# Optimization experiments

Hardware: AMD Instinct MI355X
Metric: run time of the kernel (lower is better)

The kernel has to match this reference:

```python
import jax, jax.numpy as jnp
import numpy as np

B = 4096
MAX_ATOMS = 2048  # angles_max_length + 1
EPS = 1e-12


def setup_inputs() -> dict:
    key = jax.random.key(0)
    k1, k2, k3 = jax.random.split(key, 3)
    inp = jax.random.normal(k1, (B, 3 * MAX_ATOMS), dtype=jnp.float32)
    tgt = jax.random.normal(k2, (B, 3 * MAX_ATOMS), dtype=jnp.float32)
    lengths = jax.random.randint(k3, (B,), 1, 2047, dtype=jnp.int32)
    return {"input": inp, "target": tgt, "angles_length": lengths}


def _kabsch_rmsd(inp, tgt, angles_length):
    # [B, 3*N] flat xyz -> [B, N, 3]
    b, three_n = inp.shape
    n_atoms_max = three_n // 3
    x = inp.reshape(b, n_atoms_max, 3)
    y = tgt.reshape(b, n_atoms_max, 3)
    # number of valid atoms per sample = angles_length + 1
    n_valid = (angles_length + 1).astype(x.dtype)  # [B]
    mask = (jnp.arange(n_atoms_max)[None, :] < (angles_length[:, None] + 1))
    mask = mask.astype(x.dtype)[..., None]  # [B, N, 1]
    # masked centroids
    denom = n_valid[:, None, None]
    cx = (x * mask).sum(axis=1, keepdims=True) / denom
    cy = (y * mask).sum(axis=1, keepdims=True) / denom
    xc = (x - cx) * mask
    yc = (y - cy) * mask
    # sum of squared norms of both centered point sets
    ssq = (xc * xc).sum(axis=(1, 2)) + (yc * yc).sum(axis=(1, 2))  # [B]
    # 3x3 cross-covariance per sample
    C = jnp.einsum('bni,bnj->bij', xc, yc)  # [B, 3, 3]
    U, S, Vt = jnp.linalg.svd(C)
    # Kabsch det correction (proper rotation)
    d = jnp.sign(jnp.linalg.det(U) * jnp.linalg.det(Vt))  # [B]
    tr = S[:, 0] + S[:, 1] + d * S[:, 2]
    msd = jnp.maximum(ssq - 2.0 * tr, 0.0) / n_valid
    return jnp.sqrt(msd + EPS)


def reference(input, target, angles_length):
    return _kabsch_rmsd(input, target, angles_length)
```

## Files before the change

kernel.cpp:

```cpp
#include <hip/hip_runtime.h>
#include <math.h>


#define NACC 17
#define ROWF 6144

__global__ __launch_bounds__(256) void kabsch_moments_kernel(
    const float* __restrict__ X,
    const float* __restrict__ Y,
    const int* __restrict__ L,
    float* __restrict__ WS,
    int B)
{
    const int gwave = (int)((blockIdx.x * 256u + threadIdx.x) >> 6);
    const int lane  = threadIdx.x & 63;
    if (gwave >= B) return;
    const int row = gwave;
    const int n = L[row] + 1;
    const int nIter = (n + 255) >> 8;

    const float* gX = X + (size_t)row * ROWF + (size_t)lane * 12;
    const float* gY = Y + (size_t)row * ROWF + (size_t)lane * 12;

    float v[NACC];
#pragma unroll
    for (int k = 0; k < NACC; ++k) v[k] = 0.0f;

    float4 cx0, cx1, cx2, cy0, cy1, cy2;
    {
        const float4* px = (const float4*)gX;
        const float4* py = (const float4*)gY;
        cx0 = px[0]; cx1 = px[1]; cx2 = px[2];
        cy0 = py[0]; cy1 = py[1]; cy2 = py[2];
    }

    for (int it = 0; it < nIter; ++it) {
        float4 nx0, nx1, nx2, ny0, ny1, ny2;
        const bool more = (it + 1 < nIter);
        if (more) {
            const float4* px = (const float4*)(gX + (it + 1) * 768);
            const float4* py = (const float4*)(gY + (it + 1) * 768);
            nx0 = px[0]; nx1 = px[1]; nx2 = px[2];
            ny0 = py[0]; ny1 = py[1]; ny2 = py[2];
        }

        float fx[12], fy[12];
        fx[0]=cx0.x; fx[1]=cx0.y; fx[2]=cx0.z; fx[3]=cx0.w;
        fx[4]=cx1.x; fx[5]=cx1.y; fx[6]=cx1.z; fx[7]=cx1.w;
        fx[8]=cx2.x; fx[9]=cx2.y; fx[10]=cx2.z; fx[11]=cx2.w;
        fy[0]=cy0.x; fy[1]=cy0.y; fy[2]=cy0.z; fy[3]=cy0.w;
        fy[4]=cy1.x; fy[5]=cy1.y; fy[6]=cy1.z; fy[7]=cy1.w;
        fy[8]=cy2.x; fy[9]=cy2.y; fy[10]=cy2.z; fy[11]=cy2.w;

        const int abase = it * 256 + lane * 4;
#pragma unroll
        for (int j = 0; j < 4; ++j) {
            const float msk = (abase + j < n) ? 1.0f : 0.0f;
            const float x0 = fx[3 * j + 0] * msk;
            const float x1 = fx[3 * j + 1] * msk;
            const float x2 = fx[3 * j + 2] * msk;
            const float y0 = fy[3 * j + 0] * msk;
            const float y1 = fy[3 * j + 1] * msk;
            const float y2 = fy[3 * j + 2] * msk;
            v[0] += x0; v[1] += x1; v[2] += x2;
            v[3] += y0; v[4] += y1; v[5] += y2;
            v[6] += x0 * x0 + x1 * x1 + x2 * x2;
            v[7] += y0 * y0 + y1 * y1 + y2 * y2;
            v[8]  += x0 * y0; v[9]  += x0 * y1; v[10] += x0 * y2;
            v[11] += x1 * y0; v[12] += x1 * y1; v[13] += x1 * y2;
            v[14] += x2 * y0; v[15] += x2 * y1; v[16] += x2 * y2;
        }

        if (more) {
            cx0 = nx0; cx1 = nx1; cx2 = nx2;
            cy0 = ny0; cy1 = ny1; cy2 = ny2;
        }
    }

#pragma unroll
    for (int k = 0; k < NACC; ++k) {
        float t = v[k];
        t += __shfl_down(t, 32);
        t += __shfl_down(t, 16);
        t += __shfl_down(t, 8);
        t += __shfl_down(t, 4);
        t += __shfl_down(t, 2);
        t += __shfl_down(t, 1);
        v[k] = t;
    }

    if (lane == 0) {
#pragma unroll
        for (int k = 0; k < NACC; ++k)
            WS[(size_t)k * B + row] = v[k];
    }
}

__global__ __launch_bounds__(256) void kabsch_eig_kernel(
    const float* __restrict__ WS,
    const int* __restrict__ L,
    float* __restrict__ OUT,
    int B)
{
    const int row = blockIdx.x * 256 + threadIdx.x;
    if (row >= B) return;
    const int n = L[row] + 1;

    double s[NACC];
#pragma unroll
    for (int k = 0; k < NACC; ++k)
        s[k] = (double)WS[(size_t)k * B + row];

    const double inv_n = 1.0 / (double)n;
    const double sx0 = s[0], sx1 = s[1], sx2 = s[2];
    const double sy0 = s[3], sy1 = s[4], sy2 = s[5];
    const double ssq = s[6] + s[7]
        - (sx0 * sx0 + sx1 * sx1 + sx2 * sx2) * inv_n
        - (sy0 * sy0 + sy1 * sy1 + sy2 * sy2) * inv_n;

    double C[3][3];
    C[0][0] = s[8]  - sx0 * sy0 * inv_n;
    C[0][1] = s[9]  - sx0 * sy1 * inv_n;
    C[0][2] = s[10] - sx0 * sy2 * inv_n;
    C[1][0] = s[11] - sx1 * sy0 * inv_n;
    C[1][1] = s[12] - sx1 * sy1 * inv_n;
    C[1][2] = s[13] - sx1 * sy2 * inv_n;
    C[2][0] = s[14] - sx2 * sy0 * inv_n;
    C[2][1] = s[15] - sx2 * sy1 * inv_n;
    C[2][2] = s[16] - sx2 * sy2 * inv_n;

    const double det =
          C[0][0] * (C[1][1] * C[2][2] - C[1][2] * C[2][1])
        - C[0][1] * (C[1][0] * C[2][2] - C[1][2] * C[2][0])
        + C[0][2] * (C[1][0] * C[2][1] - C[1][1] * C[2][0]);

    double A[3][3];
#pragma unroll
    for (int i = 0; i < 3; ++i)
#pragma unroll
        for (int j = 0; j < 3; ++j)
            A[i][j] = C[0][i] * C[0][j] + C[1][i] * C[1][j] + C[2][i] * C[2][j];

    const double q  = (A[0][0] + A[1][1] + A[2][2]) / 3.0;
    const double p1 = A[0][1] * A[0][1] + A[0][2] * A[0][2] + A[1][2] * A[1][2];
    const double a00 = A[0][0] - q, a11 = A[1][1] - q, a22 = A[2][2] - q;
    const double p2 = a00 * a00 + a11 * a11 + a22 * a22 + 2.0 * p1;
    const double p  = sqrt(p2 / 6.0);

    double e1, e2, e3;
    if (p < 1e-30) {
        e1 = e2 = e3 = q;
    } else {
        const double ip = 1.0 / p;
        const double b00 = a00 * ip, b11 = a11 * ip, b22 = a22 * ip;
        const double b01 = A[0][1] * ip, b02 = A[0][2] * ip, b12 = A[1][2] * ip;
        double r = 0.5 * (b00 * (b11 * b22 - b12 * b12)
                        - b01 * (b01 * b22 - b12 * b02)
                        + b02 * (b01 * b12 - b11 * b02));
        r = fmin(1.0, fmax(-1.0, r));
        const double phi = acos(r) / 3.0;
        e1 = q + 2.0 * p * cos(phi);
        e3 = q + 2.0 * p * cos(phi + 2.0 * M_PI / 3.0);
        e2 = 3.0 * q - e1 - e3;
    }

    const double S0 = sqrt(fmax(e1, 0.0));
    const double S1 = sqrt(fmax(e2, 0.0));
    const double S2 = sqrt(fmax(e3, 0.0));
    const double d  = (det > 0.0) ? 1.0 : ((det < 0.0) ? -1.0 : 0.0);
    const double tr = S0 + S1 + d * S2;

    const double msd = fmax(ssq - 2.0 * tr, 0.0) * inv_n;
    OUT[row] = (float)sqrt(msd + 1e-12);
}

extern "C" void kernel_launch(void* const* d_in, const int* in_sizes, int n_in,
                              void* d_out, int out_size, void* d_ws, size_t ws_size,
                              hipStream_t stream) {
    const float* X = (const float*)d_in[0];
    const float* Y = (const float*)d_in[1];
    const int* L = (const int*)d_in[2];
    float* OUT = (float*)d_out;
    float* WS = (float*)d_ws;

    const int B = in_sizes[2];
    const int waves_blocks = (B * 64 + 255) / 256;
    kabsch_moments_kernel<<<waves_blocks, 256, 0, stream>>>(X, Y, L, WS, B);
    kabsch_eig_kernel<<<(B + 255) / 256, 256, 0, stream>>>(WS, L, OUT, B);
}
```

Before: 201.8 us.

## Add longest-first persistent wave scheduling and fuse eigen solve into moments kernel

Adds a single-block scheduling kernel that bins rows by iteration count and emits a longest-first order, then runs a persistent kernel of 512 blocks where each wave grabs rows through a global atomic counter. The 3x3 eigen/RMSD computation is folded into lane 0 of the same wave, removing the workspace round trip and the second launch. The goal is better load balance across variable-length rows. The cost is an extra serial single-block launch, a per-row atomic, and lane-0-only double-precision math running inside the bandwidth-bound loop.

```diff
diff --git a/kernel.cpp b/kernel.cpp
--- a/kernel.cpp
+++ b/kernel.cpp
@@ -5,173 +5,198 @@
 #define NACC 17
 #define ROWF 6144
 
-__global__ __launch_bounds__(256) void kabsch_moments_kernel(
+__global__ __launch_bounds__(1024) void kabsch_schedule_kernel(
+    const int* __restrict__ L,
+    int* __restrict__ order,
+    int* __restrict__ next,
+    int B)
+{
+    __shared__ int cnt[8];
+    __shared__ int cur[8];
+    const int tid = threadIdx.x;
+
+    if (tid < 8) cnt[tid] = 0;
+    __syncthreads();
+
+    for (int row = tid; row < B; row += 1024) {
+        const int n = L[row] + 1;
+        const int b = ((n + 255) >> 8) - 1;
+        atomicAdd(&cnt[b], 1);
+    }
+    __syncthreads();
+
+    if (tid == 0) {
+        int acc = 0;
+        for (int b = 7; b >= 0; --b) {
+            cur[b] = acc;
+            acc += cnt[b];
+        }
+        *next = 0;
+    }
+    __syncthreads();
+
+    for (int row = tid; row < B; row += 1024) {
+        const int n = L[row] + 1;
+        const int b = ((n + 255) >> 8) - 1;
+        const int pos = atomicAdd(&cur[b], 1);
+        order[pos] = row;
+    }
+}
+
+__global__ __launch_bounds__(256) void kabsch_rmsd_kernel(
     const float* __restrict__ X,
     const float* __restrict__ Y,
     const int* __restrict__ L,
-    float* __restrict__ WS,
-    int B)
-{
-    const int gwave = (int)((blockIdx.x * 256u + threadIdx.x) >> 6);
-    const int lane  = threadIdx.x & 63;
-    if (gwave >= B) return;
-    const int row = gwave;
-    const int n = L[row] + 1;
-    const int nIter = (n + 255) >> 8;
-
-    const float* gX = X + (size_t)row * ROWF + (size_t)lane * 12;
-    const float* gY = Y + (size_t)row * ROWF + (size_t)lane * 12;
-
-    float v[NACC];
-#pragma unroll
-    for (int k = 0; k < NACC; ++k) v[k] = 0.0f;
-
-    float4 cx0, cx1, cx2, cy0, cy1, cy2;
-    {
-        const float4* px = (const float4*)gX;
-        const float4* py = (const float4*)gY;
-        cx0 = px[0]; cx1 = px[1]; cx2 = px[2];
-        cy0 = py[0]; cy1 = py[1]; cy2 = py[2];
-    }
-
-    for (int it = 0; it < nIter; ++it) {
-        float4 nx0, nx1, nx2, ny0, ny1, ny2;
-        const bool more = (it + 1 < nIter);
-        if (more) {
-            const float4* px = (const float4*)(gX + (it + 1) * 768);
-            const float4* py = (const float4*)(gY + (it + 1) * 768);
-            nx0 = px[0]; nx1 = px[1]; nx2 = px[2];
-            ny0 = py[0]; ny1 = py[1]; ny2 = py[2];
-        }
-
-        float fx[12], fy[12];
-        fx[0]=cx0.x; fx[1]=cx0.y; fx[2]=cx0.z; fx[3]=cx0.w;
-        fx[4]=cx1.x; fx[5]=cx1.y; fx[6]=cx1.z; fx[7]=cx1.w;
-        fx[8]=cx2.x; fx[9]=cx2.y; fx[10]=cx2.z; fx[11]=cx2.w;
-        fy[0]=cy0.x; fy[1]=cy0.y; fy[2]=cy0.z; fy[3]=cy0.w;
-        fy[4]=cy1.x; fy[5]=cy1.y; fy[6]=cy1.z; fy[7]=cy1.w;
-        fy[8]=cy2.x; fy[9]=cy2.y; fy[10]=cy2.z; fy[11]=cy2.w;
-
-        const int abase = it * 256 + lane * 4;
-#pragma unroll
-        for (int j = 0; j < 4; ++j) {
-            const float msk = (abase + j < n) ? 1.0f : 0.0f;
-            const float x0 = fx[3 * j + 0] * msk;
-            const float x1 = fx[3 * j + 1] * msk;
-            const float x2 = fx[3 * j + 2] * msk;
-            const float y0 = fy[3 * j + 0] * msk;
-            const float y1 = fy[3 * j + 1] * msk;
-            const float y2 = fy[3 * j + 2] * msk;
-            v[0] += x0; v[1] += x1; v[2] += x2;
-            v[3] += y0; v[4] += y1; v[5] += y2;
-            v[6] += x0 * x0 + x1 * x1 + x2 * x2;
-            v[7] += y0 * y0 + y1 * y1 + y2 * y2;
-            v[8]  += x0 * y0; v[9]  += x0 * y1; v[10] += x0 * y2;
-            v[11] += x1 * y0; v[12] += x1 * y1; v[13] += x1 * y2;
-            v[14] += x2 * y0; v[15] += x2 * y1; v[16] += x2 * y2;
-        }
-
-        if (more) {
-            cx0 = nx0; cx1 = nx1; cx2 = nx2;
-            cy0 = ny0; cy1 = ny1; cy2 = ny2;
-        }
-    }
-
-#pragma unroll
-    for (int k = 0; k < NACC; ++k) {
-        float t = v[k];
-        t += __shfl_down(t, 32);
-        t += __shfl_down(t, 16);
-        t += __shfl_down(t, 8);
-        t += __shfl_down(t, 4);
-        t += __shfl_down(t, 2);
-        t += __shfl_down(t, 1);
-        v[k] = t;
-    }
-
-    if (lane == 0) {
-#pragma unroll
-        for (int k = 0; k < NACC; ++k)
-            WS[(size_t)k * B + row] = v[k];
-    }
-}
-
-__global__ __launch_bounds__(256) void kabsch_eig_kernel(
-    const float* __restrict__ WS,
-    const int* __restrict__ L,
+    const int* __restrict__ order,
+    int* __restrict__ next,
     float* __restrict__ OUT,
     int B)
 {
-    const int row = blockIdx.x * 256 + threadIdx.x;
-    if (row >= B) return;
-    const int n = L[row] + 1;
-
-    double s[NACC];
-#pragma unroll
-    for (int k = 0; k < NACC; ++k)
-        s[k] = (double)WS[(size_t)k * B + row];
-
-    const double inv_n = 1.0 / (double)n;
-    const double sx0 = s[0], sx1 = s[1], sx2 = s[2];
-    const double sy0 = s[3], sy1 = s[4], sy2 = s[5];
-    const double ssq = s[6] + s[7]
-        - (sx0 * sx0 + sx1 * sx1 + sx2 * sx2) * inv_n
-        - (sy0 * sy0 + sy1 * sy1 + sy2 * sy2) * inv_n;
-
-    double C[3][3];
-    C[0][0] = s[8]  - sx0 * sy0 * inv_n;
-    C[0][1] = s[9]  - sx0 * sy1 * inv_n;
-    C[0][2] = s[10] - sx0 * sy2 * inv_n;
-    C[1][0] = s[11] - sx1 * sy0 * inv_n;
-    C[1][1] = s[12] - sx1 * sy1 * inv_n;
-    C[1][2] = s[13] - sx1 * sy2 * inv_n;
-    C[2][0] = s[14] - sx2 * sy0 * inv_n;
-    C[2][1] = s[15] - sx2 * sy1 * inv_n;
-    C[2][2] = s[16] - sx2 * sy2 * inv_n;
-
-    const double det =
-          C[0][0] * (C[1][1] * C[2][2] - C[1][2] * C[2][1])
-        - C[0][1] * (C[1][0] * C[2][2] - C[1][2] * C[2][0])
-        + C[0][2] * (C[1][0] * C[2][1] - C[1][1] * C[2][0]);
-
-    double A[3][3];
-#pragma unroll
-    for (int i = 0; i < 3; ++i)
-#pragma unroll
-        for (int j = 0; j < 3; ++j)
-            A[i][j] = C[0][i] * C[0][j] + C[1][i] * C[1][j] + C[2][i] * C[2][j];
-
-    const double q  = (A[0][0] + A[1][1] + A[2][2]) / 3.0;
-    const double p1 = A[0][1] * A[0][1] + A[0][2] * A[0][2] + A[1][2] * A[1][2];
-    const double a00 = A[0][0] - q, a11 = A[1][1] - q, a22 = A[2][2] - q;
-    const double p2 = a00 * a00 + a11 * a11 + a22 * a22 + 2.0 * p1;
-    const double p  = sqrt(p2 / 6.0);
-
-    double e1, e2, e3;
-    if (p < 1e-30) {
-        e1 = e2 = e3 = q;
-    } else {
-        const double ip = 1.0 / p;
-        const double b00 = a00 * ip, b11 = a11 * ip, b22 = a22 * ip;
-        const double b01 = A[0][1] * ip, b02 = A[0][2] * ip, b12 = A[1][2] * ip;
-        double r = 0.5 * (b00 * (b11 * b22 - b12 * b12)
-                        - b01 * (b01 * b22 - b12 * b02)
-                        + b02 * (b01 * b12 - b11 * b02));
-        r = fmin(1.0, fmax(-1.0, r));
-        const double phi = acos(r) / 3.0;
-        e1 = q + 2.0 * p * cos(phi);
-        e3 = q + 2.0 * p * cos(phi + 2.0 * M_PI / 3.0);
-        e2 = 3.0 * q - e1 - e3;
-    }
-
-    const double S0 = sqrt(fmax(e1, 0.0));
-    const double S1 = sqrt(fmax(e2, 0.0));
-    const double S2 = sqrt(fmax(e3, 0.0));
-    const double d  = (det > 0.0) ? 1.0 : ((det < 0.0) ? -1.0 : 0.0);
-    const double tr = S0 + S1 + d * S2;
-
-    const double msd = fmax(ssq - 2.0 * tr, 0.0) * inv_n;
-    OUT[row] = (float)sqrt(msd + 1e-12);
+    const int lane = threadIdx.x & 63;
+
+    for (;;) {
+        int idx = 0;
+        if (lane == 0) idx = atomicAdd(next, 1);
+        idx = __shfl(idx, 0);
+        if (idx >= B) return;
+        const int row = order[idx];
+        const int n = L[row] + 1;
+        const int nIter = (n + 255) >> 8;
+
+        const float* gX = X + (size_t)row * ROWF + (size_t)lane * 12;
+        const float* gY = Y + (size_t)row * ROWF + (size_t)lane * 12;
+
+        float v[NACC];
+#pragma unroll
+        for (int k = 0; k < NACC; ++k) v[k] = 0.0f;
+
+        float4 cx0, cx1, cx2, cy0, cy1, cy2;
+        {
+            const float4* px = (const float4*)gX;
+            const float4* py = (const float4*)gY;
+            cx0 = px[0]; cx1 = px[1]; cx2 = px[2];
+            cy0 = py[0]; cy1 = py[1]; cy2 = py[2];
+        }
+
+        for (int it = 0; it < nIter; ++it) {
+            float4 nx0, nx1, nx2, ny0, ny1, ny2;
+            const bool more = (it + 1 < nIter);
+            if (more) {
+                const float4* px = (const float4*)(gX + (it + 1) * 768);
+                const float4* py = (const float4*)(gY + (it + 1) * 768);
+                nx0 = px[0]; nx1 = px[1]; nx2 = px[2];
+                ny0 = py[0]; ny1 = py[1]; ny2 = py[2];
+            }
+
+            float fx[12], fy[12];
+            fx[0]=cx0.x; fx[1]=cx0.y; fx[2]=cx0.z; fx[3]=cx0.w;
+            fx[4]=cx1.x; fx[5]=cx1.y; fx[6]=cx1.z; fx[7]=cx1.w;
+            fx[8]=cx2.x; fx[9]=cx2.y; fx[10]=cx2.z; fx[11]=cx2.w;
+            fy[0]=cy0.x; fy[1]=cy0.y; fy[2]=cy0.z; fy[3]=cy0.w;
+            fy[4]=cy1.x; fy[5]=cy1.y; fy[6]=cy1.z; fy[7]=cy1.w;
+            fy[8]=cy2.x; fy[9]=cy2.y; fy[10]=cy2.z; fy[11]=cy2.w;
+
+            const int abase = it * 256 + lane * 4;
+#pragma unroll
+            for (int j = 0; j < 4; ++j) {
+                const float msk = (abase + j < n) ? 1.0f : 0.0f;
+                const float x0 = fx[3 * j + 0] * msk;
+                const float x1 = fx[3 * j + 1] * msk;
+                const float x2 = fx[3 * j + 2] * msk;
+                const float y0 = fy[3 * j + 0] * msk;
+                const float y1 = fy[3 * j + 1] * msk;
+                const float y2 = fy[3 * j + 2] * msk;
+                v[0] += x0; v[1] += x1; v[2] += x2;
+                v[3] += y0; v[4] += y1; v[5] += y2;
+                v[6] += x0 * x0 + x1 * x1 + x2 * x2;
+                v[7] += y0 * y0 + y1 * y1 + y2 * y2;
+                v[8]  += x0 * y0; v[9]  += x0 * y1; v[10] += x0 * y2;
+                v[11] += x1 * y0; v[12] += x1 * y1; v[13] += x1 * y2;
+                v[14] += x2 * y0; v[15] += x2 * y1; v[16] += x2 * y2;
+            }
+
+            if (more) {
+                cx0 = nx0; cx1 = nx1; cx2 = nx2;
+                cy0 = ny0; cy1 = ny1; cy2 = ny2;
+            }
+        }
+
+#pragma unroll
+        for (int k = 0; k < NACC; ++k) {
+            float t = v[k];
+            t += __shfl_down(t, 32);
+            t += __shfl_down(t, 16);
+            t += __shfl_down(t, 8);
+            t += __shfl_down(t, 4);
+            t += __shfl_down(t, 2);
+            t += __shfl_down(t, 1);
+            v[k] = t;
+        }
+
+        if (lane == 0) {
+            const double inv_n = 1.0 / (double)n;
+            const double sx0 = v[0], sx1 = v[1], sx2 = v[2];
+            const double sy0 = v[3], sy1 = v[4], sy2 = v[5];
+            const double ssq = (double)v[6] + (double)v[7]
+                - (sx0 * sx0 + sx1 * sx1 + sx2 * sx2) * inv_n
+                - (sy0 * sy0 + sy1 * sy1 + sy2 * sy2) * inv_n;
+
+            double C[3][3];
+            C[0][0] = v[8]  - sx0 * sy0 * inv_n;
+            C[0][1] = v[9]  - sx0 * sy1 * inv_n;
+            C[0][2] = v[10] - sx0 * sy2 * inv_n;
+            C[1][0] = v[11] - sx1 * sy0 * inv_n;
+            C[1][1] = v[12] - sx1 * sy1 * inv_n;
+            C[1][2] = v[13] - sx1 * sy2 * inv_n;
+            C[2][0] = v[14] - sx2 * sy0 * inv_n;
+            C[2][1] = v[15] - sx2 * sy1 * inv_n;
+            C[2][2] = v[16] - sx2 * sy2 * inv_n;
+
+            const double det =
+                  C[0][0] * (C[1][1] * C[2][2] - C[1][2] * C[2][1])
+                - C[0][1] * (C[1][0] * C[2][2] - C[1][2] * C[2][0])
+                + C[0][2] * (C[1][0] * C[2][1] - C[1][1] * C[2][0]);
+
+            double A[3][3];
+#pragma unroll
+            for (int i = 0; i < 3; ++i)
+#pragma unroll
+                for (int j = 0; j < 3; ++j)
+                    A[i][j] = C[0][i] * C[0][j] + C[1][i] * C[1][j] + C[2][i] * C[2][j];
+
+            const double q  = (A[0][0] + A[1][1] + A[2][2]) / 3.0;
+            const double p1 = A[0][1] * A[0][1] + A[0][2] * A[0][2] + A[1][2] * A[1][2];
+            const double a00 = A[0][0] - q, a11 = A[1][1] - q, a22 = A[2][2] - q;
+            const double p2 = a00 * a00 + a11 * a11 + a22 * a22 + 2.0 * p1;
+            const double p  = sqrt(p2 / 6.0);
+
+            double e1, e2, e3;
+            if (p < 1e-30) {
+                e1 = e2 = e3 = q;
+            } else {
+                const double ip = 1.0 / p;
+                const double b00 = a00 * ip, b11 = a11 * ip, b22 = a22 * ip;
+                const double b01 = A[0][1] * ip, b02 = A[0][2] * ip, b12 = A[1][2] * ip;
+                double r = 0.5 * (b00 * (b11 * b22 - b12 * b12)
+                                - b01 * (b01 * b22 - b12 * b02)
+                                + b02 * (b01 * b12 - b11 * b02));
+                r = fmin(1.0, fmax(-1.0, r));
+                const double phi = acos(r) / 3.0;
+                e1 = q + 2.0 * p * cos(phi);
+                e3 = q + 2.0 * p * cos(phi + 2.0 * M_PI / 3.0);
+                e2 = 3.0 * q - e1 - e3;
+            }
+
+            const double S0 = sqrt(fmax(e1, 0.0));
+            const double S1 = sqrt(fmax(e2, 0.0));
+            const double S2 = sqrt(fmax(e3, 0.0));
+            const double d  = (det > 0.0) ? 1.0 : ((det < 0.0) ? -1.0 : 0.0);
+            const double tr = S0 + S1 + d * S2;
+
+            const double msd = fmax(ssq - 2.0 * tr, 0.0) * inv_n;
+            OUT[row] = (float)sqrt(msd + 1e-12);
+        }
+    }
 }
 
 extern "C" void kernel_launch(void* const* d_in, const int* in_sizes, int n_in,
@@ -181,10 +206,11 @@
     const float* Y = (const float*)d_in[1];
     const int* L = (const int*)d_in[2];
     float* OUT = (float*)d_out;
-    float* WS = (float*)d_ws;
 
     const int B = in_sizes[2];
-    const int waves_blocks = (B * 64 + 255) / 256;
-    kabsch_moments_kernel<<<waves_blocks, 256, 0, stream>>>(X, Y, L, WS, B);
-    kabsch_eig_kernel<<<(B + 255) / 256, 256, 0, stream>>>(WS, L, OUT, B);
+    int* next  = (int*)d_ws;
+    int* order = (int*)d_ws + 16;
+
+    kabsch_schedule_kernel<<<1, 1024, 0, stream>>>(L, order, next, B);
+    kabsch_rmsd_kernel<<<512, 256, 0, stream>>>(X, Y, L, order, next, OUT, B);
 }
```

After: 249.5 us. 23.7% more time.

## Split each row across two waves with shared-memory combine of moments

Applied to the files above, without the earlier changes.

Each row's moment accumulation is now split between two wavefronts that take alternating 256-atom chunks, so every row gets twice the lanes and roughly half the serial iterations per wave. Partial sums are combined through shared memory after a block barrier before being written to the workspace. The kernel also adds a launch-bounds occupancy hint. The grid assumes B is even and drops the bounds check. Waves on short rows may sit idle while their partner works, and the barrier adds a sync point.

```diff
diff --git a/kernel.cpp b/kernel.cpp
--- a/kernel.cpp
+++ b/kernel.cpp
@@ -5,19 +5,21 @@
 #define NACC 17
 #define ROWF 6144
 
-__global__ __launch_bounds__(256) void kabsch_moments_kernel(
+__global__ __launch_bounds__(256, 6) void kabsch_moments_kernel(
     const float* __restrict__ X,
     const float* __restrict__ Y,
     const int* __restrict__ L,
     float* __restrict__ WS,
     int B)
 {
-    const int gwave = (int)((blockIdx.x * 256u + threadIdx.x) >> 6);
-    const int lane  = threadIdx.x & 63;
-    if (gwave >= B) return;
-    const int row = gwave;
+    const int tid  = threadIdx.x;
+    const int lane = tid & 63;
+    const int w    = tid >> 6;
+    const int half = w & 1;
+    const int row  = blockIdx.x * 2 + (w >> 1);
     const int n = L[row] + 1;
     const int nIter = (n + 255) >> 8;
+    const int cnt = (nIter > half) ? ((nIter - half + 1) >> 1) : 0;
 
     const float* gX = X + (size_t)row * ROWF + (size_t)lane * 12;
     const float* gY = Y + (size_t)row * ROWF + (size_t)lane * 12;
@@ -27,19 +29,20 @@
     for (int k = 0; k < NACC; ++k) v[k] = 0.0f;
 
     float4 cx0, cx1, cx2, cy0, cy1, cy2;
-    {
-        const float4* px = (const float4*)gX;
-        const float4* py = (const float4*)gY;
+    if (cnt > 0) {
+        const float4* px = (const float4*)(gX + half * 768);
+        const float4* py = (const float4*)(gY + half * 768);
         cx0 = px[0]; cx1 = px[1]; cx2 = px[2];
         cy0 = py[0]; cy1 = py[1]; cy2 = py[2];
     }
 
-    for (int it = 0; it < nIter; ++it) {
+    for (int s = 0; s < cnt; ++s) {
+        const int it = half + 2 * s;
+        const bool more = (s + 1 < cnt);
         float4 nx0, nx1, nx2, ny0, ny1, ny2;
-        const bool more = (it + 1 < nIter);
         if (more) {
-            const float4* px = (const float4*)(gX + (it + 1) * 768);
-            const float4* py = (const float4*)(gY + (it + 1) * 768);
+            const float4* px = (const float4*)(gX + (it + 2) * 768);
+            const float4* py = (const float4*)(gY + (it + 2) * 768);
             nx0 = px[0]; nx1 = px[1]; nx2 = px[2];
             ny0 = py[0]; ny1 = py[1]; ny2 = py[2];
         }
@@ -89,10 +92,18 @@
         v[k] = t;
     }
 
+    __shared__ float red[4][NACC];
     if (lane == 0) {
 #pragma unroll
-        for (int k = 0; k < NACC; ++k)
-            WS[(size_t)k * B + row] = v[k];
+        for (int k = 0; k < NACC; ++k) red[w][k] = v[k];
+    }
+    __syncthreads();
+
+    if (w == 0 && lane < NACC) {
+        WS[(size_t)lane * B + blockIdx.x * 2] = red[0][lane] + red[1][lane];
+    }
+    if (w == 2 && lane < NACC) {
+        WS[(size_t)lane * B + blockIdx.x * 2 + 1] = red[2][lane] + red[3][lane];
     }
 }
 
@@ -184,7 +195,6 @@
     float* WS = (float*)d_ws;
 
     const int B = in_sizes[2];
-    const int waves_blocks = (B * 64 + 255) / 256;
-    kabsch_moments_kernel<<<waves_blocks, 256, 0, stream>>>(X, Y, L, WS, B);
+    kabsch_moments_kernel<<<B / 2, 256, 0, stream>>>(X, Y, L, WS, B);
     kabsch_eig_kernel<<<(B + 255) / 256, 256, 0, stream>>>(WS, L, OUT, B);
 }
```

New measurement: 234.9 us. 1.16x slower.
